# Optimization experiments

Hardware: AMD Instinct MI355X
Metric: run time of the kernel (lower is better)

## Reference

```python
import jax, jax.numpy as jnp
import numpy as np

SEQ, BATCH = 512, 128
FEAT_CH, EMBED = 1024, 1024
N_LANG = 8  # tgt_lang_toks = [0..7]


def setup_inputs() -> dict:
    key = jax.random.key(0)
    k_feat, k_tok, k_w, k_b = jax.random.split(key, 4)
    feat = jax.random.normal(k_feat, (SEQ, BATCH, FEAT_CH), dtype=jnp.float32)
    tgt_lang_toks = jax.random.randint(k_tok, (BATCH,), 0, N_LANG, dtype=jnp.int64)
    # stacked per-language Linear params: W[l] is [embed, feat] (torch Linear layout), b[l] is [embed]
    bound = 1.0 / np.sqrt(FEAT_CH)
    W = jax.random.uniform(k_w, (N_LANG, EMBED, FEAT_CH), minval=-bound, maxval=bound, dtype=jnp.float32)
    b = jax.random.uniform(k_b, (N_LANG, EMBED), minval=-bound, maxval=bound, dtype=jnp.float32)
    return {"feat": feat, "W": W, "b": b, "tgt_lang_toks": tgt_lang_toks}


def reference(feat, W, b, tgt_lang_toks):
    # Each batch column uses the Linear of its language token. Since the
    # language token values equal their index in tgt_lang_toks=[0..7], the
    # per-group mask/gather/scatter of the original collapses to a per-batch
    # weight gather + batched matmul (grouped GEMM as dense dispatch).
    toks = tgt_lang_toks.astype(jnp.int32)
    W_sel = W[toks]          # [B, E, F]
    b_sel = b[toks]          # [B, E]
    # [S,B,F] x [B,E,F] -> [S,B,E]
    out = jnp.einsum('sbf,bef->sbe', feat, W_sel) + b_sel[None, :, :]
    return out
```

## Files before the change

kernel.cpp:

```cpp
#include <hip/hip_runtime.h>
#include <hip/hip_bf16.h>

#define SEQ   512
#define BATCH 128
#define FEAT  1024
#define EMBED 1024
#define NLANG 8

typedef __attribute__((ext_vector_type(8))) short bf16x8;
typedef __attribute__((ext_vector_type(4))) float f32x4;
typedef unsigned short ushort_t;

__device__ __forceinline__ unsigned pk2(float a, float b) {
  float2 f; f.x = a; f.y = b;
  __hip_bfloat162 h = __float22bfloat162_rn(f);
  union { __hip_bfloat162 h2; unsigned u; } cv;
  cv.h2 = h;
  return cv.u;
}

__device__ __forceinline__ bf16x8 cvt8(f32x4 lo, f32x4 hi) {
  union { bf16x8 v; unsigned u[4]; } q;
  q.u[0] = pk2(lo[0], lo[1]); q.u[1] = pk2(lo[2], lo[3]);
  q.u[2] = pk2(hi[0], hi[1]); q.u[3] = pk2(hi[2], hi[3]);
  return q.v;
}

__device__ __forceinline__ void gld16(const void* g, void* l) {
  __builtin_amdgcn_global_load_lds(
      (const __attribute__((address_space(1))) void*)g,
      (__attribute__((address_space(3))) void*)l, 16, 0, 0);
}

__global__ __launch_bounds__(256) void convert_w_kernel(
    const float* __restrict__ Wf, ushort_t* __restrict__ Wbf)
{
  const int n = (NLANG * EMBED * FEAT) / 4;
  for (int c = blockIdx.x * 256 + threadIdx.x; c < n; c += gridDim.x * 256) {
    float4 v = ((const float4*)Wf)[c];
    uint2 o; o.x = pk2(v.x, v.y); o.y = pk2(v.z, v.w);
    *(uint2*)(Wbf + ((size_t)c << 2)) = o;
  }
}

__global__ __launch_bounds__(512, 2) void grouped_gemm_fused(
    const float* __restrict__ feat,
    const ushort_t* __restrict__ Wbf,
    const float* __restrict__ bias,
    const int*   __restrict__ toks,
    float*       __restrict__ out)
{
  extern __shared__ char ldsraw[];
  float*    Af = (float*)ldsraw;
  ushort_t* Bf = (ushort_t*)(ldsraw + 98304);
  __shared__ int tokarr[128];
  __shared__ unsigned long long ballots[2][8];
  __shared__ int perm[128];
  __shared__ int rowsrc[256];

  const int tid = threadIdx.x;
  const int l   = tid & 63;
  const int w   = tid >> 6;
  const int wr  = w >> 2;
  const int wc  = w & 3;

  const int bid = blockIdx.x;
  const int L   = (bid & 7) * 128 + (bid >> 3);
  const int et  = L & 3;
  const int mt  = (L >> 7) * 32 + ((L >> 2) & 31);
  const int m0  = mt * 256;
  const int e0  = et * 256;

  if (tid < 128) tokarr[tid] = toks[tid];
  __syncthreads();
  if (tid < 128) {
    int myt = tokarr[tid];
#pragma unroll
    for (int lg = 0; lg < 8; ++lg) {
      unsigned long long bl = __ballot(myt == lg);
      if (l == 0) ballots[w][lg] = bl;
    }
  }
  __syncthreads();

  int lsel = 0, base = 0, csel = 1, boff_sel = 0;
  {
    int cum = 0, boff = 0;
#pragma unroll
    for (int lg = 0; lg < 8; ++lg) {
      int c = __popcll(ballots[0][lg]) + __popcll(ballots[1][lg]);
      int seg = c << 9;
      bool in = (m0 >= cum) && (m0 < cum + seg);
      if (in) { lsel = lg; base = cum; csel = c; boff_sel = boff; }
      cum += seg; boff += c;
    }
  }

  if (tid < 128) {
    int myt = tokarr[tid];
    unsigned long long ltm = (1ull << l) - 1ull;
    int rank = (w == 0) ? __popcll(ballots[0][myt] & ltm)
                        : __popcll(ballots[0][myt]) + __popcll(ballots[1][myt] & ltm);
    int boff2 = 0;
#pragma unroll
    for (int lg = 0; lg < 8; ++lg) {
      int c = __popcll(ballots[0][lg]) + __popcll(ballots[1][lg]);
      boff2 += (lg < myt) ? c : 0;
    }
    perm[boff2 + rank] = tid;
  }
  __syncthreads();
  if (tid < 256) {
    int local = m0 - base + tid;
    int s = local / csel;
    int j = local - s * csel;
    rowsrc[tid] = s * BATCH + perm[boff_sel + j];
  }
  __syncthreads();

  const float* aSrc[4];
#pragma unroll
  for (int i = 0; i < 4; ++i) {
    const int c    = (w * 4 + i) * 64 + l;
    const int row  = c >> 3;
    const int slot = c & 7;
    aSrc[i] = feat + (size_t)rowsrc[row] * FEAT + ((slot ^ (row & 7)) << 2);
  }
  const int aD0 = w * 1024;
  const int aD1 = aD0 + 256;
  const int aD2 = aD0 + 512;
  const int aD3 = aD0 + 768;

  const int ca  = w * 128 + l;
  const int rwB = ca >> 2;
  const int ccB = ca & 3;
  const int sB  = (rwB >> 1) & 3;
  const ushort_t* bS0 = Wbf + ((size_t)lsel * EMBED + e0 + rwB) * FEAT + ((ccB ^ sB) * 8);
  const ushort_t* bS1 = bS0 + (size_t)16 * FEAT;
  const int bD0 = (w * 128) * 8;
  const int bD1 = (w * 128 + 64) * 8;

  const int kc    = l >> 4;
  const int baseA = (wr * 128 + (l & 15)) * 32;
  const int sl0   = ((2 * kc) ^ (l & 7)) * 4;
  const int sl1   = ((2 * kc + 1) ^ (l & 7)) * 4;
  const int rB  = wc * 64 + (l & 15);
  const int bRd = rB * 32 + ((kc ^ ((rB >> 1) & 3)) * 8);

  f32x4 acc[8][4] = {};
  bf16x8 af0[4], af1[4], bfq[4];

#define STAGE_A(kt, buf)                                                   \
  do { const int _o = (kt) * 32;                                           \
    gld16(aSrc[0] + _o, Af + (buf) * 8192 + aD0);                          \
    gld16(aSrc[1] + _o, Af + (buf) * 8192 + aD1);                          \
    gld16(aSrc[2] + _o, Af + (buf) * 8192 + aD2);                          \
    gld16(aSrc[3] + _o, Af + (buf) * 8192 + aD3); } while (0)
#define STAGE_B(kt, buf)                                                   \
  do { const int _o = (kt) * 32;                                           \
    gld16(bS0 + _o, Bf + (buf) * 8192 + bD0);                              \
    gld16(bS1 + _o, Bf + (buf) * 8192 + bD1); } while (0)

#define PH0(g, rbuf, sbuf, DOSTAGE)                                        \
  do {                                                                     \
    const float*    Ab_ = Af + (rbuf) * 8192;                              \
    const ushort_t* Bb_ = Bf + (rbuf) * 8192;                              \
    _Pragma("unroll") for (int mf = 0; mf < 4; ++mf) {                     \
      f32x4 lo_ = *(const f32x4*)(Ab_ + baseA + mf * 512 + sl0);           \
      f32x4 hi_ = *(const f32x4*)(Ab_ + baseA + mf * 512 + sl1);           \
      af0[mf] = cvt8(lo_, hi_);                                            \
    }                                                                      \
    _Pragma("unroll") for (int nf = 0; nf < 4; ++nf)                       \
      bfq[nf] = *(const bf16x8*)(Bb_ + bRd + nf * 512);                    \
    if (DOSTAGE) { STAGE_A((g) + 2, sbuf); }                               \
    __builtin_amdgcn_sched_barrier(0);                                     \
    __builtin_amdgcn_s_barrier();                                          \
    asm volatile("s_waitcnt lgkmcnt(0)" ::: "memory");                     \
    __builtin_amdgcn_sched_barrier(0);                                     \
    __builtin_amdgcn_s_setprio(1);                                         \
    _Pragma("unroll") for (int mf = 0; mf < 4; ++mf)                       \
        _Pragma("unroll") for (int nf = 0; nf < 4; ++nf)                   \
            acc[mf][nf] = __builtin_amdgcn_mfma_f32_16x16x32_bf16(         \
                af0[mf], bfq[nf], acc[mf][nf], 0, 0, 0);                   \
    __builtin_amdgcn_s_setprio(0);                                         \
    __builtin_amdgcn_s_barrier();                                          \
  } while (0)

#define PH1(g, rbuf, sbuf, DOSTAGE, WAIT)                                  \
  do {                                                                     \
    const float* Ab_ = Af + (rbuf) * 8192;                                 \
    _Pragma("unroll") for (int mf = 0; mf < 4; ++mf) {                     \
      f32x4 lo_ = *(const f32x4*)(Ab_ + baseA + (mf + 4) * 512 + sl0);     \
      f32x4 hi_ = *(const f32x4*)(Ab_ + baseA + (mf + 4) * 512 + sl1);     \
      af1[mf] = cvt8(lo_, hi_);                                            \
    }                                                                      \
    if (DOSTAGE) { STAGE_B((g) + 2, sbuf); }                               \
    __builtin_amdgcn_sched_barrier(0);                                     \
    __builtin_amdgcn_s_barrier();                                          \
    asm volatile("s_waitcnt lgkmcnt(0)" ::: "memory");                     \
    __builtin_amdgcn_sched_barrier(0);                                     \
    __builtin_amdgcn_s_setprio(1);                                         \
    _Pragma("unroll") for (int mf = 0; mf < 4; ++mf)                       \
        _Pragma("unroll") for (int nf = 0; nf < 4; ++nf)                   \
            acc[mf + 4][nf] = __builtin_amdgcn_mfma_f32_16x16x32_bf16(     \
                af1[mf], bfq[nf], acc[mf + 4][nf], 0, 0, 0);               \
    __builtin_amdgcn_s_setprio(0);                                         \
    asm volatile(WAIT ::: "memory");                                       \
    __builtin_amdgcn_s_barrier();                                          \
  } while (0)

  STAGE_A(0, 0); STAGE_B(0, 0);
  STAGE_A(1, 1); STAGE_B(1, 1);
  asm volatile("s_waitcnt vmcnt(6)" ::: "memory");
  __builtin_amdgcn_s_barrier();
  __builtin_amdgcn_sched_barrier(0);

#pragma unroll 1
  for (int gg = 0; gg < 10; ++gg) {
    const int g = gg * 3;
    PH0(g + 0, 0, 2, true);  PH1(g + 0, 0, 2, true, "s_waitcnt vmcnt(6)");
    PH0(g + 1, 1, 0, true);  PH1(g + 1, 1, 0, true, "s_waitcnt vmcnt(6)");
    PH0(g + 2, 2, 1, true);  PH1(g + 2, 2, 1, true, "s_waitcnt vmcnt(6)");
  }
  PH0(30, 0, 0, false); PH1(30, 0, 0, false, "s_waitcnt vmcnt(0)");
  PH0(31, 1, 0, false); PH1(31, 1, 0, false, "s_nop 0");

#undef PH0
#undef PH1
#undef STAGE_A
#undef STAGE_B

  const int col = l & 15;
  const int r4  = (l >> 4) * 4;
  float bvv[4];
#pragma unroll
  for (int nf = 0; nf < 4; ++nf)
    bvv[nf] = bias[lsel * EMBED + e0 + wc * 64 + nf * 16 + col];
#pragma unroll
  for (int mf = 0; mf < 8; ++mf) {
#pragma unroll
    for (int j = 0; j < 4; ++j) {
      const size_t ro = (size_t)rowsrc[wr * 128 + mf * 16 + r4 + j] * EMBED;
#pragma unroll
      for (int nf = 0; nf < 4; ++nf)
        out[ro + e0 + wc * 64 + nf * 16 + col] = acc[mf][nf][j] + bvv[nf];
    }
  }
}

__global__ __launch_bounds__(256, 2) void grouped_proj_fused(
    const float* __restrict__ feat, const float* __restrict__ Wt,
    const float* __restrict__ bias, const int* __restrict__ toks,
    float* __restrict__ out)
{
  __shared__ uint4 As[1024];
  __shared__ uint4 Bs[1024];
  __shared__ int tokarr[128];
  __shared__ unsigned long long ballots[2][8];
  __shared__ int perm[128];
  __shared__ int rowsrc[128];

  const int tid  = threadIdx.x;
  const int lane = tid & 63;
  const int wv   = tid >> 6;
  const int wr   = wv >> 1;
  const int wc   = wv & 1;
  const int bid = blockIdx.x;
  const int xcd = bid & 7;
  const int sq  = bid >> 3;
  const int et  = sq & 7;
  const int mt  = (sq >> 3) * 8 + xcd;
  const int m0  = mt * 128;
  const int e0  = et * 128;

  if (tid < 128) tokarr[tid] = toks[tid];
  __syncthreads();
  if (tid < 128) {
    int myt = tokarr[tid];
#pragma unroll
    for (int lg = 0; lg < 8; ++lg) {
      unsigned long long bl = __ballot(myt == lg);
      if (lane == 0) ballots[wv][lg] = bl;
    }
  }
  __syncthreads();
  int lsel = 0, base = 0, csel = 1, boff_sel = 0;
  {
    int cum = 0, boff = 0;
#pragma unroll
    for (int lg = 0; lg < 8; ++lg) {
      int c = __popcll(ballots[0][lg]) + __popcll(ballots[1][lg]);
      int seg = c << 9;
      bool in = (m0 >= cum) && (m0 < cum + seg);
      if (in) { lsel = lg; base = cum; csel = c; boff_sel = boff; }
      cum += seg; boff += c;
    }
  }
  if (tid < 128) {
    int myt = tokarr[tid];
    unsigned long long ltm = (1ull << lane) - 1ull;
    int rank = (wv == 0) ? __popcll(ballots[0][myt] & ltm)
                         : __popcll(ballots[0][myt]) + __popcll(ballots[1][myt] & ltm);
    int boff2 = 0;
#pragma unroll
    for (int lg = 0; lg < 8; ++lg) {
      int c = __popcll(ballots[0][lg]) + __popcll(ballots[1][lg]);
      boff2 += (lg < myt) ? c : 0;
    }
    perm[boff2 + rank] = tid;
  }
  __syncthreads();
  if (tid < 128) {
    int local = m0 - base + tid;
    int s = local / csel;
    int j = local - s * csel;
    rowsrc[tid] = s * BATCH + perm[boff_sel + j];
  }
  __syncthreads();

  int slot_i[4];
  const float* aptr[4];
  const float* bptr[4];
#pragma unroll
  for (int it = 0; it < 4; ++it) {
    int c    = it * 256 + tid;
    int kg   = c & 7;
    int row  = c >> 3;
    int ksub = kg & 3;
    int kk   = kg >> 2;
    int frag = row >> 4;
    slot_i[it] = (kk * 8 + frag) * 64 + ((row & 15) ^ (ksub << 1) ^ kk) + ksub * 16;
    aptr[it] = feat + (size_t)rowsrc[row] * FEAT + kg * 8;
    bptr[it] = Wt + ((size_t)lsel * EMBED + e0 + row) * FEAT + kg * 8;
  }

  f32x4 acc[4][4] = {};
  for (int k0 = 0; k0 < FEAT; k0 += 64) {
    __syncthreads();
#pragma unroll
    for (int it = 0; it < 4; ++it) {
      float4 alo = *(const float4*)(aptr[it] + k0);
      float4 ahi = *(const float4*)(aptr[it] + k0 + 4);
      uint4 av;
      av.x = pk2(alo.x, alo.y); av.y = pk2(alo.z, alo.w);
      av.z = pk2(ahi.x, ahi.y); av.w = pk2(ahi.z, ahi.w);
      As[slot_i[it]] = av;
      float4 blo = *(const float4*)(bptr[it] + k0);
      float4 bhi = *(const float4*)(bptr[it] + k0 + 4);
      uint4 bv;
      bv.x = pk2(blo.x, blo.y); bv.y = pk2(blo.z, blo.w);
      bv.z = pk2(bhi.x, bhi.y); bv.w = pk2(bhi.z, bhi.w);
      Bs[slot_i[it]] = bv;
    }
    __syncthreads();
#pragma unroll
    for (int kk = 0; kk < 2; ++kk) {
      const int ksr = lane >> 4;
      const int sw  = ((lane & 15) ^ (ksr << 1) ^ kk) + ksr * 16;
      bf16x8 af[4], bfr[4];
#pragma unroll
      for (int mi = 0; mi < 4; ++mi)
        af[mi] = ((const bf16x8*)As)[(kk * 8 + wr * 4 + mi) * 64 + sw];
#pragma unroll
      for (int ni = 0; ni < 4; ++ni)
        bfr[ni] = ((const bf16x8*)Bs)[(kk * 8 + wc * 4 + ni) * 64 + sw];
#pragma unroll
      for (int mi = 0; mi < 4; ++mi)
#pragma unroll
        for (int ni = 0; ni < 4; ++ni)
          acc[mi][ni] = __builtin_amdgcn_mfma_f32_16x16x32_bf16(
              af[mi], bfr[ni], acc[mi][ni], 0, 0, 0);
    }
  }

  const int col = lane & 15;
  const int r0  = (lane >> 4) * 4;
  float bvv[4];
#pragma unroll
  for (int ni = 0; ni < 4; ++ni)
    bvv[ni] = bias[lsel * EMBED + e0 + wc * 64 + ni * 16 + col];
#pragma unroll
  for (int mi = 0; mi < 4; ++mi) {
#pragma unroll
    for (int j = 0; j < 4; ++j) {
      const size_t ro = (size_t)rowsrc[wr * 64 + mi * 16 + r0 + j] * EMBED;
#pragma unroll
      for (int ni = 0; ni < 4; ++ni)
        out[ro + e0 + wc * 64 + ni * 16 + col] = acc[mi][ni][j] + bvv[ni];
    }
  }
}

extern "C" void kernel_launch(void* const* d_in, const int* in_sizes, int n_in,
                              void* d_out, int out_size, void* d_ws, size_t ws_size,
                              hipStream_t stream) {
  const float* feat = (const float*)d_in[0];
  const float* W    = (const float*)d_in[1];
  const float* bias = (const float*)d_in[2];
  const int*   toks = (const int*)d_in[3];
  float* out = (float*)d_out;

  const size_t wbf_bytes = (size_t)NLANG * EMBED * FEAT * 2;

  if (ws_size >= wbf_bytes) {
    ushort_t* Wbf = (ushort_t*)d_ws;
    convert_w_kernel<<<512, 256, 0, stream>>>(W, Wbf);
    (void)hipFuncSetAttribute((const void*)grouped_gemm_fused,
                              hipFuncAttributeMaxDynamicSharedMemorySize, 147456);
    const int nblk = (SEQ * BATCH / 256) * (EMBED / 256);
    grouped_gemm_fused<<<nblk, 512, 147456, stream>>>(feat, Wbf, bias, toks, out);
  } else {
    grouped_proj_fused<<<(SEQ * BATCH / 128) * (EMBED / 128), 256, 0, stream>>>(
        feat, W, bias, toks, out);
  }
}
```

Baseline: 241.5 us.

## Convert A tile to bf16 once via register staging instead of per-wave fp32 LDS reads

Activations are now loaded from global into registers, converted to bf16 once per block, and written to a double-buffered bf16 LDS tile, replacing direct fp32 global-to-LDS loads that every wave had to re-read and convert. This reduces LDS footprint (fp32 A buffers to bf16), LDS read bandwidth and redundant conversion work. The two half-phases per k-step are merged into one granule with a single barrier, so each k-step syncs once instead of twice. The cost is extra VGPRs for in-flight A registers, plus VALU conversion and LDS writes on the critical path of each step.

```diff
diff --git a/kernel.cpp b/kernel.cpp
--- a/kernel.cpp
+++ b/kernel.cpp
@@ -19,10 +19,10 @@
   return cv.u;
 }
 
-__device__ __forceinline__ bf16x8 cvt8(f32x4 lo, f32x4 hi) {
+__device__ __forceinline__ bf16x8 cvt8(float4 lo, float4 hi) {
   union { bf16x8 v; unsigned u[4]; } q;
-  q.u[0] = pk2(lo[0], lo[1]); q.u[1] = pk2(lo[2], lo[3]);
-  q.u[2] = pk2(hi[0], hi[1]); q.u[3] = pk2(hi[2], hi[3]);
+  q.u[0] = pk2(lo.x, lo.y); q.u[1] = pk2(lo.z, lo.w);
+  q.u[2] = pk2(hi.x, hi.y); q.u[3] = pk2(hi.z, hi.w);
   return q.v;
 }
 
@@ -51,8 +51,8 @@
     float*       __restrict__ out)
 {
   extern __shared__ char ldsraw[];
-  float*    Af = (float*)ldsraw;
-  ushort_t* Bf = (ushort_t*)(ldsraw + 98304);
+  ushort_t* Af = (ushort_t*)ldsraw;
+  ushort_t* Bf = (ushort_t*)(ldsraw + 32768);
   __shared__ int tokarr[128];
   __shared__ unsigned long long ballots[2][8];
   __shared__ int perm[128];
@@ -118,18 +118,13 @@
   }
   __syncthreads();
 
-  const float* aSrc[4];
-#pragma unroll
-  for (int i = 0; i < 4; ++i) {
-    const int c    = (w * 4 + i) * 64 + l;
-    const int row  = c >> 3;
-    const int slot = c & 7;
-    aSrc[i] = feat + (size_t)rowsrc[row] * FEAT + ((slot ^ (row & 7)) << 2);
-  }
-  const int aD0 = w * 1024;
-  const int aD1 = aD0 + 256;
-  const int aD2 = aD0 + 512;
-  const int aD3 = aD0 + 768;
+  const int arow = tid >> 1;
+  const int ah   = tid & 1;
+  const float* aSrcP = feat + (size_t)rowsrc[arow] * FEAT + ah * 16;
+  const int sAw     = (arow >> 1) & 3;
+  const int wchunk0 = arow * 4 + ((2 * ah) ^ sAw);
+  const int wchunk1 = arow * 4 + ((2 * ah + 1) ^ sAw);
+  float4 ar0, ar1, ar2, ar3;
 
   const int ca  = w * 128 + l;
   const int rwB = ca >> 2;
@@ -140,94 +135,78 @@
   const int bD0 = (w * 128) * 8;
   const int bD1 = (w * 128 + 64) * 8;
 
-  const int kc    = l >> 4;
-  const int baseA = (wr * 128 + (l & 15)) * 32;
-  const int sl0   = ((2 * kc) ^ (l & 7)) * 4;
-  const int sl1   = ((2 * kc + 1) ^ (l & 7)) * 4;
+  const int kc  = l >> 4;
+  const int rA  = wr * 128 + (l & 15);
+  const int aRd = rA * 32 + ((kc ^ ((rA >> 1) & 3)) * 8);
   const int rB  = wc * 64 + (l & 15);
   const int bRd = rB * 32 + ((kc ^ ((rB >> 1) & 3)) * 8);
 
   f32x4 acc[8][4] = {};
-  bf16x8 af0[4], af1[4], bfq[4];
-
-#define STAGE_A(kt, buf)                                                   \
-  do { const int _o = (kt) * 32;                                           \
-    gld16(aSrc[0] + _o, Af + (buf) * 8192 + aD0);                          \
-    gld16(aSrc[1] + _o, Af + (buf) * 8192 + aD1);                          \
-    gld16(aSrc[2] + _o, Af + (buf) * 8192 + aD2);                          \
-    gld16(aSrc[3] + _o, Af + (buf) * 8192 + aD3); } while (0)
+
+#define LOAD_A(kt)                                                         \
+  do { const float* _p = aSrcP + (kt) * 32;                                \
+    ar0 = *(const float4*)(_p);      ar1 = *(const float4*)(_p + 4);       \
+    ar2 = *(const float4*)(_p + 8);  ar3 = *(const float4*)(_p + 12); } while (0)
+#define WRITE_A(buf)                                                       \
+  do { bf16x8* _wp = (bf16x8*)(Af + (buf) * 8192);                         \
+    _wp[wchunk0] = cvt8(ar0, ar1);                                         \
+    _wp[wchunk1] = cvt8(ar2, ar3); } while (0)
 #define STAGE_B(kt, buf)                                                   \
   do { const int _o = (kt) * 32;                                           \
     gld16(bS0 + _o, Bf + (buf) * 8192 + bD0);                              \
     gld16(bS1 + _o, Bf + (buf) * 8192 + bD1); } while (0)
 
-#define PH0(g, rbuf, sbuf, DOSTAGE)                                        \
+#define GRAN(G, J, DOCVT, DOSTAGE, ENDWAIT, ENDBAR)                        \
   do {                                                                     \
-    const float*    Ab_ = Af + (rbuf) * 8192;                              \
-    const ushort_t* Bb_ = Bf + (rbuf) * 8192;                              \
-    _Pragma("unroll") for (int mf = 0; mf < 4; ++mf) {                     \
-      f32x4 lo_ = *(const f32x4*)(Ab_ + baseA + mf * 512 + sl0);           \
-      f32x4 hi_ = *(const f32x4*)(Ab_ + baseA + mf * 512 + sl1);           \
-      af0[mf] = cvt8(lo_, hi_);                                            \
-    }                                                                      \
+    if (DOCVT) { WRITE_A(((J) + 1) & 1); }                                 \
+    if (DOSTAGE) { LOAD_A((G) + 2); STAGE_B((G) + 2, ((J) + 2) % 3); }     \
+    __builtin_amdgcn_sched_barrier(0);                                     \
+    const ushort_t* Ar_ = Af + ((J) & 1) * 8192;                           \
+    const ushort_t* Br_ = Bf + ((J) % 3) * 8192;                           \
+    bf16x8 af[8], bfq[4];                                                  \
+    _Pragma("unroll") for (int mf = 0; mf < 8; ++mf)                       \
+        af[mf] = *(const bf16x8*)(Ar_ + aRd + mf * 512);                   \
     _Pragma("unroll") for (int nf = 0; nf < 4; ++nf)                       \
-      bfq[nf] = *(const bf16x8*)(Bb_ + bRd + nf * 512);                    \
-    if (DOSTAGE) { STAGE_A((g) + 2, sbuf); }                               \
-    __builtin_amdgcn_sched_barrier(0);                                     \
-    __builtin_amdgcn_s_barrier();                                          \
+        bfq[nf] = *(const bf16x8*)(Br_ + bRd + nf * 512);                  \
     asm volatile("s_waitcnt lgkmcnt(0)" ::: "memory");                     \
     __builtin_amdgcn_sched_barrier(0);                                     \
     __builtin_amdgcn_s_setprio(1);                                         \
-    _Pragma("unroll") for (int mf = 0; mf < 4; ++mf)                       \
+    _Pragma("unroll") for (int mf = 0; mf < 8; ++mf)                       \
         _Pragma("unroll") for (int nf = 0; nf < 4; ++nf)                   \
             acc[mf][nf] = __builtin_amdgcn_mfma_f32_16x16x32_bf16(         \
-                af0[mf], bfq[nf], acc[mf][nf], 0, 0, 0);                   \
+                af[mf], bfq[nf], acc[mf][nf], 0, 0, 0);                    \
     __builtin_amdgcn_s_setprio(0);                                         \
-    __builtin_amdgcn_s_barrier();                                          \
+    asm volatile(ENDWAIT ::: "memory");                                    \
+    if (ENDBAR) { __builtin_amdgcn_s_barrier();                            \
+                  __builtin_amdgcn_sched_barrier(0); }                     \
   } while (0)
 
-#define PH1(g, rbuf, sbuf, DOSTAGE, WAIT)                                  \
-  do {                                                                     \
-    const float* Ab_ = Af + (rbuf) * 8192;                                 \
-    _Pragma("unroll") for (int mf = 0; mf < 4; ++mf) {                     \
-      f32x4 lo_ = *(const f32x4*)(Ab_ + baseA + (mf + 4) * 512 + sl0);     \
-      f32x4 hi_ = *(const f32x4*)(Ab_ + baseA + (mf + 4) * 512 + sl1);     \
-      af1[mf] = cvt8(lo_, hi_);                                            \
-    }                                                                      \
-    if (DOSTAGE) { STAGE_B((g) + 2, sbuf); }                               \
-    __builtin_amdgcn_sched_barrier(0);                                     \
-    __builtin_amdgcn_s_barrier();                                          \
-    asm volatile("s_waitcnt lgkmcnt(0)" ::: "memory");                     \
-    __builtin_amdgcn_sched_barrier(0);                                     \
-    __builtin_amdgcn_s_setprio(1);                                         \
-    _Pragma("unroll") for (int mf = 0; mf < 4; ++mf)                       \
-        _Pragma("unroll") for (int nf = 0; nf < 4; ++nf)                   \
-            acc[mf + 4][nf] = __builtin_amdgcn_mfma_f32_16x16x32_bf16(     \
-                af1[mf], bfq[nf], acc[mf + 4][nf], 0, 0, 0);               \
-    __builtin_amdgcn_s_setprio(0);                                         \
-    asm volatile(WAIT ::: "memory");                                       \
-    __builtin_amdgcn_s_barrier();                                          \
-  } while (0)
-
-  STAGE_A(0, 0); STAGE_B(0, 0);
-  STAGE_A(1, 1); STAGE_B(1, 1);
+  LOAD_A(0);
+  STAGE_B(0, 0);
+  WRITE_A(0);
+  LOAD_A(1);
+  STAGE_B(1, 1);
+  __builtin_amdgcn_sched_barrier(0);
+  asm volatile("s_waitcnt lgkmcnt(0)" ::: "memory");
   asm volatile("s_waitcnt vmcnt(6)" ::: "memory");
   __builtin_amdgcn_s_barrier();
   __builtin_amdgcn_sched_barrier(0);
 
 #pragma unroll 1
-  for (int gg = 0; gg < 10; ++gg) {
-    const int g = gg * 3;
-    PH0(g + 0, 0, 2, true);  PH1(g + 0, 0, 2, true, "s_waitcnt vmcnt(6)");
-    PH0(g + 1, 1, 0, true);  PH1(g + 1, 1, 0, true, "s_waitcnt vmcnt(6)");
-    PH0(g + 2, 2, 1, true);  PH1(g + 2, 2, 1, true, "s_waitcnt vmcnt(6)");
-  }
-  PH0(30, 0, 0, false); PH1(30, 0, 0, false, "s_waitcnt vmcnt(0)");
-  PH0(31, 1, 0, false); PH1(31, 1, 0, false, "s_nop 0");
-
-#undef PH0
-#undef PH1
-#undef STAGE_A
+  for (int gb = 0; gb < 30; gb += 6) {
+    GRAN(gb + 0, 0, true, true, "s_waitcnt vmcnt(6)", true);
+    GRAN(gb + 1, 1, true, true, "s_waitcnt vmcnt(6)", true);
+    GRAN(gb + 2, 2, true, true, "s_waitcnt vmcnt(6)", true);
+    GRAN(gb + 3, 3, true, true, "s_waitcnt vmcnt(6)", true);
+    GRAN(gb + 4, 4, true, true, "s_waitcnt vmcnt(6)", true);
+    GRAN(gb + 5, 5, true, true, "s_waitcnt vmcnt(6)", true);
+  }
+  GRAN(30, 0, true, false, "s_waitcnt vmcnt(0)", true);
+  GRAN(31, 1, false, false, "s_nop 0", false);
+
+#undef GRAN
+#undef LOAD_A
+#undef WRITE_A
 #undef STAGE_B
 
   const int col = l & 15;
@@ -406,9 +385,9 @@
     ushort_t* Wbf = (ushort_t*)d_ws;
     convert_w_kernel<<<512, 256, 0, stream>>>(W, Wbf);
     (void)hipFuncSetAttribute((const void*)grouped_gemm_fused,
-                              hipFuncAttributeMaxDynamicSharedMemorySize, 147456);
+                              hipFuncAttributeMaxDynamicSharedMemorySize, 81920);
     const int nblk = (SEQ * BATCH / 256) * (EMBED / 256);
-    grouped_gemm_fused<<<nblk, 512, 147456, stream>>>(feat, Wbf, bias, toks, out);
+    grouped_gemm_fused<<<nblk, 512, 81920, stream>>>(feat, Wbf, bias, toks, out);
   } else {
     grouped_proj_fused<<<(SEQ * BATCH / 128) * (EMBED / 128), 256, 0, stream>>>(
         feat, W, bias, toks, out);
```

New measurement: 300.5 us. 1.24x slower.
